# Optimization experiments

Measured on AMD Instinct MI355X. Metric: run time of the kernel, lower is better.

Reference implementation:

```python
import jax, jax.numpy as jnp
import numpy as np

B, T = 4, 1024
H, C, DK, DV = 12, 4096, 64, 64
DIM = H * DK  # 768


def setup_inputs() -> dict:
    key = jax.random.key(0)
    k1, k2, k3 = jax.random.split(key, 3)
    x = jax.random.normal(k1, (B, T, DIM), dtype=jnp.float32)
    # key_embed initialized with kaiming_uniform in torch; uniform in [-bound, bound]
    bound = float(np.sqrt(3.0) * np.sqrt(2.0) / np.sqrt(C * DK))
    key_embed = jax.random.uniform(k2, (H, C, DK), minval=-bound, maxval=bound, dtype=jnp.float32)
    values = jax.random.normal(k3, (H, C, DV), dtype=jnp.float32)
    mask = jnp.ones((B, T), dtype=jnp.int32)
    return {"x": x, "mask": mask, "key_embed": key_embed, "values": values, "key_optim": 0}


def reference(x, mask, key_embed, values, key_optim):
    # x: [b, t, h*dk]; key_embed: [h, c, dk]; values: [h, c, dv]
    b, t, _ = x.shape
    h, c, dk = key_embed.shape
    dv = values.shape[-1]
    x = x.astype(jnp.float32)
    # 'b t (h d) -> h (b t) d'
    xh = x.reshape(b, t, h, dk).transpose(2, 0, 1, 3).reshape(h, b * t, dk)
    # squared-L2 nearest codebook entry (argmax of -cdist == argmin of squared dist)
    x2 = jnp.sum(xh * xh, axis=-1, keepdims=True)          # [h, n, 1]
    e2 = jnp.sum(key_embed * key_embed, axis=-1)           # [h, c]
    dots = jnp.einsum('hnd,hcd->hnc', xh, key_embed)       # [h, n, c]
    d2 = x2 - 2.0 * dots + e2[:, None, :]                  # [h, n, c]
    ind = jnp.argmin(d2, axis=-1)                          # [h, n]
    # gather per-head learned values: values[h, ind[h, n], :]
    memories = jnp.take_along_axis(values, ind[..., None], axis=1)  # [h, n, dv]
    # 'h (b t) dv -> b t (h dv)'  (decoder == 'mlp')
    memories = memories.transpose(1, 0, 2).reshape(b, t, h * dv)
    return memories
```

## Files before the change

kernel.cpp:

```cpp
#include <hip/hip_runtime.h>


#define HEADS 12
#define CODES 4096
#define DKI   64
#define DVI   64
#define DIMX  768
#define TAUS  7.68e-3f
#define WLCAP 32768

typedef short bf16x8 __attribute__((ext_vector_type(8)));
typedef _Float16 f16x8 __attribute__((ext_vector_type(8)));
typedef float f32x16 __attribute__((ext_vector_type(16)));

__device__ __forceinline__ unsigned short f2bf(float f) {
    unsigned int u = __float_as_uint(f);
    return (unsigned short)((u + 0x7fff + ((u >> 16) & 1)) >> 16);
}
__device__ __forceinline__ unsigned short f2h(float f) {
    _Float16 h = (_Float16)f;
    unsigned short u;
    __builtin_memcpy(&u, &h, 2);
    return u;
}
__device__ __forceinline__ f16x8 as_f16x8(uint4 v) {
    union { uint4 u; f16x8 h; } c; c.u = v; return c.h;
}

__device__ __forceinline__ float np_sumsq64(const float* __restrict__ a) {
#pragma clang fp contract(off)
    float r[8];
#pragma unroll
    for (int j = 0; j < 8; ++j) r[j] = a[j] * a[j];
#pragma unroll
    for (int i = 8; i < 64; i += 8)
#pragma unroll
        for (int j = 0; j < 8; ++j) r[j] += a[i + j] * a[i + j];
    return ((r[0] + r[1]) + (r[2] + r[3])) + ((r[4] + r[5]) + (r[6] + r[7]));
}

__device__ __forceinline__ float np_dot64(const float* __restrict__ xx,
                                          const float* __restrict__ ee) {
#pragma clang fp contract(off)
    float S0 = 0.f, S1 = 0.f, S2 = 0.f, S3 = 0.f;
#pragma unroll
    for (int t = 0; t < 64; t += 16) {
        float p[16];
#pragma unroll
        for (int j = 0; j < 16; ++j) p[j] = xx[t + j] * ee[t + j];
        S0 = p[0] + (p[4] + (p[8]  + (p[12] + S0)));
        S1 = p[1] + (p[5] + (p[9]  + (p[13] + S1)));
        S2 = p[2] + (p[6] + (p[10] + (p[14] + S2)));
        S3 = p[3] + (p[7] + (p[11] + (p[15] + S3)));
    }
    return (S0 + S1) + (S2 + S3);
}

__global__ __launch_bounds__(256) void prep_ke(const float* __restrict__ ke,
                                               uint4* __restrict__ EhT,
                                               float* __restrict__ e2np,
                                               unsigned short* __restrict__ m2bf,
                                               int* __restrict__ wl_count) {
    __shared__ float sq[32][64];
    __shared__ float rr[32][8];
    const int t = threadIdx.x;
    if (blockIdx.x == 0 && t < 2) wl_count[t] = 0;
    const int p = t >> 5, cw = t & 31;
    const int idx = blockIdx.x * 32 + cw;

    float er[8];
    {
        const float4* p4 = reinterpret_cast<const float4*>(
            ke + (size_t)idx * DKI + p * 8);
        float4 v0 = p4[0], v1 = p4[1];
        er[0] = v0.x; er[1] = v0.y; er[2] = v0.z; er[3] = v0.w;
        er[4] = v1.x; er[5] = v1.y; er[6] = v1.z; er[7] = v1.w;
    }
    {
#pragma clang fp contract(off)
#pragma unroll
        for (int j = 0; j < 8; ++j) sq[cw][p * 8 + j] = er[j] * er[j];
    }
    __syncthreads();
    {
#pragma clang fp contract(off)
        float r = sq[cw][p];
#pragma unroll
        for (int k = 1; k < 8; ++k) r = r + sq[cw][k * 8 + p];
        rr[cw][p] = r;
    }
    __syncthreads();
    const int h = idx >> 12, c = idx & 4095;
    const int half = c >> 11, gg = (c & 2047) >> 5;
    const int pair = h * 2 + half;
    if (p == 0) {
#pragma clang fp contract(off)
        float e2 = ((rr[cw][0] + rr[cw][1]) + (rr[cw][2] + rr[cw][3])) +
                   ((rr[cw][4] + rr[cw][5]) + (rr[cw][6] + rr[cw][7]));
        e2np[idx] = e2;
        m2bf[(size_t)pair * 2048 + (c & 2047)] = f2bf(-32.f * e2);
    }

    unsigned int hb[8];
#pragma unroll
    for (int j = 0; j < 8; ++j)
        hb[j] = f2h(er[j] * 64.f);
    uint4 hv;
    hv.x = hb[0] | (hb[1] << 16); hv.y = hb[2] | (hb[3] << 16);
    hv.z = hb[4] | (hb[5] << 16); hv.w = hb[6] | (hb[7] << 16);
    EhT[((size_t)(pair * 64 + gg) * 8 + p) * 32 + cw] = hv;
}

#define MERGE3(v1o, i1o, v2o, i2o, v3o,                                   \
               a1, j1, a2, j2, a3, b1, k1, b2, k2, b3)                    \
    {                                                                     \
        bool t1 = (b1) > (a1);                                            \
        float _l1 = t1 ? (a1) : (b1);  int _k1 = t1 ? (j1) : (k1);        \
        (v1o) = t1 ? (b1) : (a1);      (i1o) = t1 ? (k1) : (j1);          \
        float _s2 = t1 ? (b2) : (a2);  int _u2 = t1 ? (k2) : (j2);        \
        bool t2 = _s2 > _l1;                                              \
        (v2o) = t2 ? _s2 : _l1;        (i2o) = t2 ? _u2 : _k1;            \
        float _l2 = t2 ? _l1 : _s2;                                       \
        float _s3 = t2 ? (t1 ? (b3) : (a3)) : (t1 ? (a2) : (b2));         \
        bool t3 = _s3 > _l2;                                              \
        (v3o) = t3 ? _s3 : _l2;                                           \
    }

__global__ __launch_bounds__(256, 3) void dkvb_pass1(
        const float* __restrict__ x,
        const char* __restrict__ EhT,
        const unsigned short* __restrict__ m2bf,
        const float* __restrict__ values,
        int* __restrict__ wl_count,
        int* __restrict__ wl,
        int* __restrict__ wlc,
        int* __restrict__ wlf,
        unsigned long long* __restrict__ res,
        int* __restrict__ pcnt,
        float* __restrict__ out) {
    __shared__ float sb1[4][32], sb2[4][32], sb3[4][32];
    __shared__ int   sbi[4][32];
    __shared__ int   fin[32];

    const int tid  = threadIdx.x;
    const int h    = blockIdx.x % 12;
    const int qb   = blockIdx.x / 12;
    const int w    = tid >> 6;
    const int lane = tid & 63;
    const int col  = lane & 31;
    const int kh   = lane >> 5;
    const int q0   = qb * 32;
    const int pair = h * 2 + (w >> 1);

    const float* xrow = x + (size_t)(q0 + col) * DIMX + h * DKI;
    f16x8 ah[4];
#pragma unroll
    for (int t = 0; t < 4; ++t) {
        const float* p = xrow + t * 16 + kh * 8;
        float4 v0 = *reinterpret_cast<const float4*>(p);
        float4 v1 = *reinterpret_cast<const float4*>(p + 4);
        f16x8 hv;
        hv[0] = (_Float16)v0.x; hv[1] = (_Float16)v0.y;
        hv[2] = (_Float16)v0.z; hv[3] = (_Float16)v0.w;
        hv[4] = (_Float16)v1.x; hv[5] = (_Float16)v1.y;
        hv[6] = (_Float16)v1.z; hv[7] = (_Float16)v1.w;
        ah[t] = hv;
    }
    const bf16x8 am2 = (bf16x8){(short)(kh ? 0 : 0x3F80), 0, 0, 0, 0, 0, 0, 0};

    const char* gE = EhT + (size_t)pair * 262144 + (size_t)(w & 1) * 131072
                   + (size_t)kh * 512 + (size_t)col * 16;
    const unsigned short* gm = m2bf + (size_t)pair * 2048
                             + (size_t)(w & 1) * 1024 + col;

    f32x16 zacc;
#pragma unroll
    for (int r = 0; r < 16; ++r) zacc[r] = 0.f;

    float bv[16], bv2[16], bv3[16];
#pragma unroll
    for (int r = 0; r < 16; ++r) { bv[r] = -1e30f; bv2[r] = -1e30f; bv3[r] = -1e30f; }

    auto LOADF = [&](int i, uint4& e0, uint4& e1, uint4& e2, uint4& e3,
                     unsigned short& mA) {
        const char* p = gE + (size_t)i * 4096;
        e0 = *reinterpret_cast<const uint4*>(p);
        e1 = *reinterpret_cast<const uint4*>(p + 1024);
        e2 = *reinterpret_cast<const uint4*>(p + 2048);
        e3 = *reinterpret_cast<const uint4*>(p + 3072);
        mA = gm[i * 32];
    };
    auto COMPUTE = [&](int i, uint4 e0, uint4 e1, uint4 e2, uint4 e3,
                       unsigned short mA) {
        bf16x8 bm = (bf16x8){(short)(kh ? 0 : mA), 0, 0, 0, 0, 0, 0, 0};
        f32x16 acc;
        acc = __builtin_amdgcn_mfma_f32_32x32x16_bf16(am2,   bm,          zacc, 0, 0, 0);
        acc = __builtin_amdgcn_mfma_f32_32x32x16_f16 (ah[0], as_f16x8(e0), acc, 0, 0, 0);
        acc = __builtin_amdgcn_mfma_f32_32x32x16_f16 (ah[1], as_f16x8(e1), acc, 0, 0, 0);
        acc = __builtin_amdgcn_mfma_f32_32x32x16_f16 (ah[2], as_f16x8(e2), acc, 0, 0, 0);
        acc = __builtin_amdgcn_mfma_f32_32x32x16_f16 (ah[3], as_f16x8(e3), acc, 0, 0, 0);
        unsigned enc = (unsigned)i;
#pragma unroll
        for (int r = 0; r < 16; ++r) {
            float sp = __uint_as_float(
                (__float_as_uint(acc[r]) & 0xFFFFFFC0u) | enc);
            bv3[r] = __builtin_amdgcn_fmed3f(bv3[r], sp, bv2[r]);
            bv2[r] = __builtin_amdgcn_fmed3f(bv2[r], sp, bv[r]);
            bv[r]  = fmaxf(bv[r], sp);
        }
    };

    uint4 A0, A1, A2, A3, B0, B1, B2, B3, C0, C1, C2, C3;
    unsigned short Am, Bm, Cm;
    LOADF(0, A0, A1, A2, A3, Am);
    LOADF(1, B0, B1, B2, B3, Bm);
#pragma unroll 1
    for (int i = 0; i < 30; i += 3) {
        LOADF(i + 2, C0, C1, C2, C3, Cm);
        COMPUTE(i, A0, A1, A2, A3, Am);
        LOADF(i + 3, A0, A1, A2, A3, Am);
        COMPUTE(i + 1, B0, B1, B2, B3, Bm);
        LOADF(i + 4, B0, B1, B2, B3, Bm);
        COMPUTE(i + 2, C0, C1, C2, C3, Cm);
    }
    COMPUTE(30, A0, A1, A2, A3, Am);
    COMPUTE(31, B0, B1, B2, B3, Bm);

    int bi1[16], bi2[16];
#pragma unroll
    for (int r = 0; r < 16; ++r) {
        bi1[r] = (int)(__float_as_uint(bv[r])  & 63u) * 32 + col + w * 1024;
        bi2[r] = (int)(__float_as_uint(bv2[r]) & 63u) * 32 + col + w * 1024;
    }
#pragma unroll
    for (int r = 0; r < 16; ++r) {
#pragma unroll
        for (int m = 1; m <= 16; m <<= 1) {
            float p1 = __shfl_xor(bv[r],  m, 64);
            float p2 = __shfl_xor(bv2[r], m, 64);
            float p3 = __shfl_xor(bv3[r], m, 64);
            int   q1 = __shfl_xor(bi1[r], m, 64);
            int   q2 = __shfl_xor(bi2[r], m, 64);
            bool t1 = (p1 > bv[r]) || (p1 == bv[r] && q1 < bi1[r]);
            float w1 = t1 ? p1 : bv[r];   int j1 = t1 ? q1 : bi1[r];
            float l1 = t1 ? bv[r] : p1;   int k1 = t1 ? bi1[r] : q1;
            float s2 = t1 ? p2 : bv2[r];  int u2 = t1 ? q2 : bi2[r];
            bool t2 = s2 > l1;
            float w2 = t2 ? s2 : l1;      int j2 = t2 ? u2 : k1;
            float l2 = t2 ? l1 : s2;
            float s3 = t2 ? (t1 ? p3 : bv3[r]) : (t1 ? bv2[r] : p2);
            bool t3 = s3 > l2;
            float w3 = t3 ? s3 : l2;
            bv[r] = w1; bi1[r] = j1;
            bv2[r] = w2; bi2[r] = j2;
            bv3[r] = w3;
        }
    }
    if (col == 0) {
#pragma unroll
        for (int r = 0; r < 16; ++r) {
            int row = (r & 3) + 8 * (r >> 2) + 4 * kh;
            sb1[w][row] = bv[r];
            sb2[w][row] = bv2[r];
            sb3[w][row] = bv3[r];
            sbi[w][row] = (bi1[r] << 16) | bi2[r];
        }
    }
    __syncthreads();

    if (tid < 32) {
        float v1[4], v2[4], v3[4]; int i1[4], i2[4];
#pragma unroll
        for (int qd = 0; qd < 4; ++qd) {
            v1[qd] = sb1[qd][tid]; v2[qd] = sb2[qd][tid]; v3[qd] = sb3[qd][tid];
            int pk = sbi[qd][tid];
            i1[qd] = (pk >> 16) & 0xffff; i2[qd] = pk & 0xffff;
        }
        float m1a, m2a, m3a, m1b, m2b, m3b, V1, V2, V3;
        int j1a, j2a, j1b, j2b, I1, I2;
        MERGE3(m1a, j1a, m2a, j2a, m3a,
               v1[0], i1[0], v2[0], i2[0], v3[0],
               v1[1], i1[1], v2[1], i2[1], v3[1]);
        MERGE3(m1b, j1b, m2b, j2b, m3b,
               v1[2], i1[2], v2[2], i2[2], v3[2],
               v1[3], i1[3], v2[3], i2[3], v3[3]);
        MERGE3(V1, I1, V2, I2, V3,
               m1a, j1a, m2a, j2a, m3a,
               m1b, j1b, m2b, j2b, m3b);
        fin[tid] = I1;
        if (V1 - V2 < TAUS) {
            if (V1 - V3 < TAUS) {
                int slot = atomicAdd(wl_count + 1, 1);
                if (slot < WLCAP) {
                    wlf[slot]  = (h << 16) | (q0 + tid);
                    res[slot]  = ~0ULL;
                    pcnt[slot] = 0;
                }
            } else {
                int slot = atomicAdd(wl_count, 1);
                if (slot < WLCAP) {
                    wl[slot]  = (h << 16) | (q0 + tid);
                    wlc[slot] = (I1 << 16) | I2;
                }
            }
        }
    }
    __syncthreads();

#pragma unroll
    for (int k = 0; k < 2; ++k) {
        int f   = tid + k * 256;
        int row = f >> 4;
        int cl  = (f & 15) << 2;
        int idx = fin[row];
        float4 v = *reinterpret_cast<const float4*>(
            values + (size_t)h * CODES * DVI + (size_t)idx * DVI + cl);
        *reinterpret_cast<float4*>(
            out + (size_t)(q0 + row) * DIMX + h * DVI + cl) = v;
    }
}

__global__ __launch_bounds__(256) void post_check(const float* __restrict__ x,
                                                  const float* __restrict__ ke,
                                                  const float* __restrict__ e2np,
                                                  const float* __restrict__ values,
                                                  const int* __restrict__ wl_count,
                                                  const int* __restrict__ wl,
                                                  const int* __restrict__ wlc,
                                                  const int* __restrict__ wlf,
                                                  unsigned long long* __restrict__ res,
                                                  int* __restrict__ pcnt,
                                                  float* __restrict__ out) {
    __shared__ float xs[4][DKI];
    const int t = threadIdx.x, w = t >> 6, lane = t & 63;
    int cnt0 = wl_count[0]; if (cnt0 > WLCAP) cnt0 = WLCAP;
    int cnt1 = wl_count[1]; if (cnt1 > WLCAP) cnt1 = WLCAP;
    const int total = cnt0 + cnt1 * 8;

    for (int item = blockIdx.x * 4 + w; item < total; item += gridDim.x * 4) {
        if (item < cnt0) {
            int ent = wl[item];
            int h = ent >> 16, nq = ent & 0xffff;
            int cp = wlc[item];
            if (lane < 16) {
                float4 v = *reinterpret_cast<const float4*>(
                    x + (size_t)nq * DIMX + h * DKI + lane * 4);
                *reinterpret_cast<float4*>(&xs[w][lane * 4]) = v;
            }
            asm volatile("s_waitcnt lgkmcnt(0)" ::: "memory");
            __builtin_amdgcn_sched_barrier(0);

            int i1 = (cp >> 16) & 0xffff, i2 = cp & 0xffff;
            float d2 = 0.f;
            if (lane < 2) {
                int myc = lane ? i2 : i1;
                float er[DKI];
                const float4* p = reinterpret_cast<const float4*>(
                    ke + ((size_t)h * CODES + myc) * DKI);
#pragma unroll
                for (int i = 0; i < DKI / 4; ++i) {
                    float4 v = p[i];
                    er[i * 4 + 0] = v.x; er[i * 4 + 1] = v.y;
                    er[i * 4 + 2] = v.z; er[i * 4 + 3] = v.w;
                }
                float x2 = np_sumsq64(xs[w]);
                float dot = np_dot64(xs[w], er);
                {
#pragma clang fp contract(off)
                    d2 = (x2 - 2.0f * dot) + e2np[h * CODES + myc];
                }
            }
            float dA = __shfl(d2, 0, 64);
            float dB = __shfl(d2, 1, 64);
            int win = (dB < dA || (dB == dA && i2 < i1)) ? i2 : i1;
            if (lane < 16) {
                float4 v = *reinterpret_cast<const float4*>(
                    values + ((size_t)h * CODES + win) * DVI + lane * 4);
                *reinterpret_cast<float4*>(
                    out + (size_t)nq * DIMX + h * DVI + lane * 4) = v;
            }
        } else {
            const int j = item - cnt0;
            const int e = j >> 3, part = j & 7;
            const int ent = wlf[e];
            const int h = ent >> 16, nq = ent & 0xffff;
            if (lane < 16) {
                float4 v = *reinterpret_cast<const float4*>(
                    x + (size_t)nq * DIMX + h * DKI + lane * 4);
                *reinterpret_cast<float4*>(&xs[w][lane * 4]) = v;
            }
            asm volatile("s_waitcnt lgkmcnt(0)" ::: "memory");
            __builtin_amdgcn_sched_barrier(0);

            float x2 = np_sumsq64(xs[w]);
            unsigned long long best = ~0ULL;
#pragma unroll 1
            for (int it = 0; it < 8; ++it) {
                int c = part * 512 + it * 64 + lane;
                float er[DKI];
                const float4* p = reinterpret_cast<const float4*>(
                    ke + ((size_t)h * CODES + c) * DKI);
#pragma unroll
                for (int i = 0; i < DKI / 4; ++i) {
                    float4 v = p[i];
                    er[i * 4 + 0] = v.x; er[i * 4 + 1] = v.y;
                    er[i * 4 + 2] = v.z; er[i * 4 + 3] = v.w;
                }
                float dot = np_dot64(xs[w], er);
                float d2;
                {
#pragma clang fp contract(off)
                    d2 = (x2 - 2.0f * dot) + e2np[h * CODES + c];
                }
                unsigned u = __float_as_uint(d2);
                unsigned key = (u & 0x80000000u) ? ~u : (u | 0x80000000u);
                unsigned long long pk =
                    ((unsigned long long)key << 32) | (unsigned)c;
                best = pk < best ? pk : best;
            }
#pragma unroll
            for (int m = 1; m <= 32; m <<= 1) {
                unsigned long long o =
                    (unsigned long long)__shfl_xor((long long)best, m, 64);
                best = o < best ? o : best;
            }
            int lastflag = 0;
            if (lane == 0) {
                atomicMin(res + e, best);
                __threadfence();
                lastflag = (atomicAdd(pcnt + e, 1) == 7);
            }
            lastflag = __shfl(lastflag, 0, 64);
            if (lastflag) {
                unsigned long long fin = 0;
                if (lane == 0) {
                    __threadfence();
                    fin = atomicMin(res + e, ~0ULL);
                }
                int win = (int)(__shfl((long long)fin, 0, 64) & 0xFFFFFFFFLL);
                if (lane < 16) {
                    float4 v = *reinterpret_cast<const float4*>(
                        values + ((size_t)h * CODES + win) * DVI + lane * 4);
                    *reinterpret_cast<float4*>(
                        out + (size_t)nq * DIMX + h * DVI + lane * 4) = v;
                }
            }
        }
    }
}

extern "C" void kernel_launch(void* const* d_in, const int* in_sizes, int n_in,
                              void* d_out, int out_size, void* d_ws, size_t ws_size,
                              hipStream_t stream) {
    const float* x      = (const float*)d_in[0];
    const float* ke     = (const float*)d_in[2];
    const float* values = (const float*)d_in[3];
    float* out = (float*)d_out;

    char* ws = (char*)d_ws;
    float* e2np          = (float*)ws;          ws += (size_t)HEADS * CODES * 4;
    unsigned short* m2bf = (unsigned short*)ws; ws += (size_t)HEADS * 2 * 2048 * 2;
    int*   wl_count      = (int*)ws;            ws += 64;
    int*   wl            = (int*)ws;            ws += (size_t)WLCAP * 4;
    int*   wlc           = (int*)ws;            ws += (size_t)WLCAP * 4;
    int*   wlf           = (int*)ws;            ws += (size_t)WLCAP * 4;
    unsigned long long* res = (unsigned long long*)ws; ws += (size_t)WLCAP * 8;
    int*   pcnt          = (int*)ws;            ws += (size_t)WLCAP * 4;
    char*  EhT           = ws;                  ws += (size_t)HEADS * CODES * 128;

    prep_ke<<<dim3(HEADS * CODES / 32), dim3(256), 0, stream>>>(
        ke, (uint4*)EhT, e2np, m2bf, wl_count);
    dkvb_pass1<<<dim3(1536), dim3(256), 0, stream>>>(
        x, EhT, m2bf, values, wl_count, wl, wlc, wlf, res, pcnt, out);
    post_check<<<dim3(1024), dim3(256), 0, stream>>>(
        x, ke, e2np, values, wl_count, wl, wlc, wlf, res, pcnt, out);
}
```

Before: 192.6 us.

## Switch pass1 distance MFMA from 32x32x16 to 16x16x32 tiles

```diff
diff --git a/kernel.cpp b/kernel.cpp
--- a/kernel.cpp
+++ b/kernel.cpp
@@ -11,7 +11,7 @@
 
 typedef short bf16x8 __attribute__((ext_vector_type(8)));
 typedef _Float16 f16x8 __attribute__((ext_vector_type(8)));
-typedef float f32x16 __attribute__((ext_vector_type(16)));
+typedef float f32x4 __attribute__((ext_vector_type(4)));
 
 __device__ __forceinline__ unsigned short f2bf(float f) {
     unsigned int u = __float_as_uint(f);
@@ -126,7 +126,7 @@
         (v3o) = t3 ? _s3 : _l2;                                           \
     }
 
-__global__ __launch_bounds__(256, 3) void dkvb_pass1(
+__global__ __launch_bounds__(256, 4) void dkvb_pass1(
         const float* __restrict__ x,
         const char* __restrict__ EhT,
         const unsigned short* __restrict__ m2bf,
@@ -147,124 +147,141 @@
     const int qb   = blockIdx.x / 12;
     const int w    = tid >> 6;
     const int lane = tid & 63;
-    const int col  = lane & 31;
-    const int kh   = lane >> 5;
+    const int cl16 = lane & 15;
+    const int kg   = lane >> 4;
     const int q0   = qb * 32;
     const int pair = h * 2 + (w >> 1);
-
-    const float* xrow = x + (size_t)(q0 + col) * DIMX + h * DKI;
-    f16x8 ah[4];
-#pragma unroll
-    for (int t = 0; t < 4; ++t) {
-        const float* p = xrow + t * 16 + kh * 8;
-        float4 v0 = *reinterpret_cast<const float4*>(p);
-        float4 v1 = *reinterpret_cast<const float4*>(p + 4);
-        f16x8 hv;
-        hv[0] = (_Float16)v0.x; hv[1] = (_Float16)v0.y;
-        hv[2] = (_Float16)v0.z; hv[3] = (_Float16)v0.w;
-        hv[4] = (_Float16)v1.x; hv[5] = (_Float16)v1.y;
-        hv[6] = (_Float16)v1.z; hv[7] = (_Float16)v1.w;
-        ah[t] = hv;
-    }
-    const bf16x8 am2 = (bf16x8){(short)(kh ? 0 : 0x3F80), 0, 0, 0, 0, 0, 0, 0};
-
-    const char* gE = EhT + (size_t)pair * 262144 + (size_t)(w & 1) * 131072
-                   + (size_t)kh * 512 + (size_t)col * 16;
+    const int qoff = (w >> 1) * 2048 + (w & 1) * 1024;
+
+    f16x8 ah[2][2];
+#pragma unroll
+    for (int T = 0; T < 2; ++T) {
+        const float* xrow = x + (size_t)(q0 + T * 16 + cl16) * DIMX + h * DKI;
+#pragma unroll
+        for (int t = 0; t < 2; ++t) {
+            const float* p = xrow + t * 32 + kg * 8;
+            float4 v0 = *reinterpret_cast<const float4*>(p);
+            float4 v1 = *reinterpret_cast<const float4*>(p + 4);
+            f16x8 hv;
+            hv[0] = (_Float16)v0.x; hv[1] = (_Float16)v0.y;
+            hv[2] = (_Float16)v0.z; hv[3] = (_Float16)v0.w;
+            hv[4] = (_Float16)v1.x; hv[5] = (_Float16)v1.y;
+            hv[6] = (_Float16)v1.z; hv[7] = (_Float16)v1.w;
+            ah[T][t] = hv;
+        }
+    }
+    const bf16x8 am2 = (bf16x8){(short)(kg ? 0 : 0x3F80), 0, 0, 0, 0, 0, 0, 0};
+
+    const char* gE = EhT + (size_t)(pair * 64 + (w & 1) * 32) * 4096
+                   + (size_t)kg * 512 + (size_t)cl16 * 16;
     const unsigned short* gm = m2bf + (size_t)pair * 2048
-                             + (size_t)(w & 1) * 1024 + col;
-
-    f32x16 zacc;
-#pragma unroll
-    for (int r = 0; r < 16; ++r) zacc[r] = 0.f;
-
-    float bv[16], bv2[16], bv3[16];
-#pragma unroll
-    for (int r = 0; r < 16; ++r) { bv[r] = -1e30f; bv2[r] = -1e30f; bv3[r] = -1e30f; }
-
-    auto LOADF = [&](int i, uint4& e0, uint4& e1, uint4& e2, uint4& e3,
-                     unsigned short& mA) {
-        const char* p = gE + (size_t)i * 4096;
-        e0 = *reinterpret_cast<const uint4*>(p);
-        e1 = *reinterpret_cast<const uint4*>(p + 1024);
-        e2 = *reinterpret_cast<const uint4*>(p + 2048);
-        e3 = *reinterpret_cast<const uint4*>(p + 3072);
-        mA = gm[i * 32];
+                             + (size_t)(w & 1) * 1024 + cl16;
+
+    f32x4 zacc;
+#pragma unroll
+    for (int r = 0; r < 4; ++r) zacc[r] = 0.f;
+
+    float bv[2][4], bv2[2][4], bv3[2][4];
+#pragma unroll
+    for (int T = 0; T < 2; ++T)
+#pragma unroll
+        for (int r = 0; r < 4; ++r) {
+            bv[T][r] = -1e30f; bv2[T][r] = -1e30f; bv3[T][r] = -1e30f;
+        }
+
+    auto LOADF = [&](int i, uint4& b0, uint4& b1, unsigned short& mA) {
+        const char* p = gE + (size_t)(i >> 1) * 4096 + (size_t)(i & 1) * 256;
+        b0 = *reinterpret_cast<const uint4*>(p);
+        b1 = *reinterpret_cast<const uint4*>(p + 2048);
+        mA = gm[i * 16];
     };
-    auto COMPUTE = [&](int i, uint4 e0, uint4 e1, uint4 e2, uint4 e3,
-                       unsigned short mA) {
-        bf16x8 bm = (bf16x8){(short)(kh ? 0 : mA), 0, 0, 0, 0, 0, 0, 0};
-        f32x16 acc;
-        acc = __builtin_amdgcn_mfma_f32_32x32x16_bf16(am2,   bm,          zacc, 0, 0, 0);
-        acc = __builtin_amdgcn_mfma_f32_32x32x16_f16 (ah[0], as_f16x8(e0), acc, 0, 0, 0);
-        acc = __builtin_amdgcn_mfma_f32_32x32x16_f16 (ah[1], as_f16x8(e1), acc, 0, 0, 0);
-        acc = __builtin_amdgcn_mfma_f32_32x32x16_f16 (ah[2], as_f16x8(e2), acc, 0, 0, 0);
-        acc = __builtin_amdgcn_mfma_f32_32x32x16_f16 (ah[3], as_f16x8(e3), acc, 0, 0, 0);
+    auto COMPUTE = [&](int i, uint4 b0, uint4 b1, unsigned short mA) {
+        bf16x8 bm = (bf16x8){(short)(kg ? 0 : mA), 0, 0, 0, 0, 0, 0, 0};
         unsigned enc = (unsigned)i;
 #pragma unroll
-        for (int r = 0; r < 16; ++r) {
-            float sp = __uint_as_float(
-                (__float_as_uint(acc[r]) & 0xFFFFFFC0u) | enc);
-            bv3[r] = __builtin_amdgcn_fmed3f(bv3[r], sp, bv2[r]);
-            bv2[r] = __builtin_amdgcn_fmed3f(bv2[r], sp, bv[r]);
-            bv[r]  = fmaxf(bv[r], sp);
+        for (int T = 0; T < 2; ++T) {
+            f32x4 acc;
+            acc = __builtin_amdgcn_mfma_f32_16x16x32_bf16(am2, bm, zacc, 0, 0, 0);
+            acc = __builtin_amdgcn_mfma_f32_16x16x32_f16(ah[T][0], as_f16x8(b0),
+                                                         acc, 0, 0, 0);
+            acc = __builtin_amdgcn_mfma_f32_16x16x32_f16(ah[T][1], as_f16x8(b1),
+                                                         acc, 0, 0, 0);
+#pragma unroll
+            for (int r = 0; r < 4; ++r) {
+                float sp = __uint_as_float(
+                    (__float_as_uint(acc[r]) & 0xFFFFFFC0u) | enc);
+                bv3[T][r] = __builtin_amdgcn_fmed3f(bv3[T][r], sp, bv2[T][r]);
+                bv2[T][r] = __builtin_amdgcn_fmed3f(bv2[T][r], sp, bv[T][r]);
+                bv[T][r]  = fmaxf(bv[T][r], sp);
+            }
         }
     };
 
-    uint4 A0, A1, A2, A3, B0, B1, B2, B3, C0, C1, C2, C3;
+    uint4 A0, A1, B0, B1, C0, C1;
     unsigned short Am, Bm, Cm;
-    LOADF(0, A0, A1, A2, A3, Am);
-    LOADF(1, B0, B1, B2, B3, Bm);
+    LOADF(0, A0, A1, Am);
+    LOADF(1, B0, B1, Bm);
 #pragma unroll 1
-    for (int i = 0; i < 30; i += 3) {
-        LOADF(i + 2, C0, C1, C2, C3, Cm);
-        COMPUTE(i, A0, A1, A2, A3, Am);
-        LOADF(i + 3, A0, A1, A2, A3, Am);
-        COMPUTE(i + 1, B0, B1, B2, B3, Bm);
-        LOADF(i + 4, B0, B1, B2, B3, Bm);
-        COMPUTE(i + 2, C0, C1, C2, C3, Cm);
-    }
-    COMPUTE(30, A0, A1, A2, A3, Am);
-    COMPUTE(31, B0, B1, B2, B3, Bm);
-
-    int bi1[16], bi2[16];
-#pragma unroll
-    for (int r = 0; r < 16; ++r) {
-        bi1[r] = (int)(__float_as_uint(bv[r])  & 63u) * 32 + col + w * 1024;
-        bi2[r] = (int)(__float_as_uint(bv2[r]) & 63u) * 32 + col + w * 1024;
-    }
-#pragma unroll
-    for (int r = 0; r < 16; ++r) {
-#pragma unroll
-        for (int m = 1; m <= 16; m <<= 1) {
-            float p1 = __shfl_xor(bv[r],  m, 64);
-            float p2 = __shfl_xor(bv2[r], m, 64);
-            float p3 = __shfl_xor(bv3[r], m, 64);
-            int   q1 = __shfl_xor(bi1[r], m, 64);
-            int   q2 = __shfl_xor(bi2[r], m, 64);
-            bool t1 = (p1 > bv[r]) || (p1 == bv[r] && q1 < bi1[r]);
-            float w1 = t1 ? p1 : bv[r];   int j1 = t1 ? q1 : bi1[r];
-            float l1 = t1 ? bv[r] : p1;   int k1 = t1 ? bi1[r] : q1;
-            float s2 = t1 ? p2 : bv2[r];  int u2 = t1 ? q2 : bi2[r];
-            bool t2 = s2 > l1;
-            float w2 = t2 ? s2 : l1;      int j2 = t2 ? u2 : k1;
-            float l2 = t2 ? l1 : s2;
-            float s3 = t2 ? (t1 ? p3 : bv3[r]) : (t1 ? bv2[r] : p2);
-            bool t3 = s3 > l2;
-            float w3 = t3 ? s3 : l2;
-            bv[r] = w1; bi1[r] = j1;
-            bv2[r] = w2; bi2[r] = j2;
-            bv3[r] = w3;
-        }
-    }
-    if (col == 0) {
-#pragma unroll
-        for (int r = 0; r < 16; ++r) {
-            int row = (r & 3) + 8 * (r >> 2) + 4 * kh;
-            sb1[w][row] = bv[r];
-            sb2[w][row] = bv2[r];
-            sb3[w][row] = bv3[r];
-            sbi[w][row] = (bi1[r] << 16) | bi2[r];
-        }
+    for (int i = 0; i < 60; i += 3) {
+        LOADF(i + 2, C0, C1, Cm);
+        COMPUTE(i, A0, A1, Am);
+        LOADF(i + 3, A0, A1, Am);
+        COMPUTE(i + 1, B0, B1, Bm);
+        LOADF(i + 4, B0, B1, Bm);
+        COMPUTE(i + 2, C0, C1, Cm);
+    }
+    LOADF(62, C0, C1, Cm);
+    COMPUTE(60, A0, A1, Am);
+    LOADF(63, A0, A1, Am);
+    COMPUTE(61, B0, B1, Bm);
+    COMPUTE(62, C0, C1, Cm);
+    COMPUTE(63, A0, A1, Am);
+
+    int bi1[2][4], bi2[2][4];
+#pragma unroll
+    for (int T = 0; T < 2; ++T)
+#pragma unroll
+        for (int r = 0; r < 4; ++r) {
+            bi1[T][r] = (int)(__float_as_uint(bv[T][r])  & 63u) * 16 + cl16 + qoff;
+            bi2[T][r] = (int)(__float_as_uint(bv2[T][r]) & 63u) * 16 + cl16 + qoff;
+        }
+#pragma unroll
+    for (int T = 0; T < 2; ++T)
+#pragma unroll
+        for (int r = 0; r < 4; ++r) {
+#pragma unroll
+            for (int m = 1; m <= 8; m <<= 1) {
+                float p1 = __shfl_xor(bv[T][r],  m, 64);
+                float p2 = __shfl_xor(bv2[T][r], m, 64);
+                float p3 = __shfl_xor(bv3[T][r], m, 64);
+                int   q1 = __shfl_xor(bi1[T][r], m, 64);
+                int   q2 = __shfl_xor(bi2[T][r], m, 64);
+                bool t1 = (p1 > bv[T][r]) || (p1 == bv[T][r] && q1 < bi1[T][r]);
+                float w1 = t1 ? p1 : bv[T][r];   int j1 = t1 ? q1 : bi1[T][r];
+                float l1 = t1 ? bv[T][r] : p1;   int k1 = t1 ? bi1[T][r] : q1;
+                float s2 = t1 ? p2 : bv2[T][r];  int u2 = t1 ? q2 : bi2[T][r];
+                bool t2 = s2 > l1;
+                float w2 = t2 ? s2 : l1;         int j2 = t2 ? u2 : k1;
+                float l2 = t2 ? l1 : s2;
+                float s3 = t2 ? (t1 ? p3 : bv3[T][r]) : (t1 ? bv2[T][r] : p2);
+                bool t3 = s3 > l2;
+                float w3 = t3 ? s3 : l2;
+                bv[T][r] = w1; bi1[T][r] = j1;
+                bv2[T][r] = w2; bi2[T][r] = j2;
+                bv3[T][r] = w3;
+            }
+        }
+    if (cl16 == 0) {
+#pragma unroll
+        for (int T = 0; T < 2; ++T)
+#pragma unroll
+            for (int r = 0; r < 4; ++r) {
+                int row = T * 16 + kg * 4 + r;
+                sb1[w][row] = bv[T][r];
+                sb2[w][row] = bv2[T][r];
+                sb3[w][row] = bv3[T][r];
+                sbi[w][row] = (bi1[T][r] << 16) | bi2[T][r];
+            }
     }
     __syncthreads();
 
```

Result: faster. 173.8 us (-9.8%).
